# Kernel tuning notes

Hardware: AMD Instinct MI355X
Metric: run time of the kernel (lower is better)

The kernel has to match this reference:

```python
import jax, jax.numpy as jnp
import numpy as np

N_NODES = 50000
N_EDGES = 1600000
IN_FEAT = 256
OUT_FEAT = 64


def setup_inputs() -> dict:
    key = jax.random.key(0)
    k1, k2, k3, k4, k5, k6 = jax.random.split(key, 6)
    feat = jax.random.normal(k1, (N_NODES, IN_FEAT), dtype=jnp.float32)
    edge_src = jax.random.randint(k2, (N_EDGES,), 0, N_NODES, dtype=jnp.int32)
    edge_dst = jax.random.randint(k3, (N_EDGES,), 0, N_NODES, dtype=jnp.int32)
    edge_weight = jax.random.uniform(k4, (N_EDGES,), dtype=jnp.float32)
    # Xavier-uniform init as in reset_parameters
    bound = float(np.sqrt(6.0 / (IN_FEAT + OUT_FEAT)))
    W_self = jax.random.uniform(k5, (IN_FEAT, OUT_FEAT), minval=-bound, maxval=bound, dtype=jnp.float32)
    W_neigh = jax.random.uniform(k6, (IN_FEAT, OUT_FEAT), minval=-bound, maxval=bound, dtype=jnp.float32)
    return {"feat": feat, "edge_src": edge_src, "edge_dst": edge_dst,
            "edge_weight": edge_weight, "W_self": W_self, "W_neigh": W_neigh}


def reference(feat, edge_src, edge_dst, edge_weight, W_self, W_neigh):
    # neigh_feat = spmm(adj, feat): row dst aggregates weighted neighbors src
    gathered = feat[edge_src] * edge_weight[:, None]          # [E, in_feat]
    neigh_feat = jax.ops.segment_sum(gathered, edge_dst, num_segments=N_NODES)  # [N, in_feat]
    self_feat = feat @ W_self                                 # [N, out_feat]
    neigh_feat = neigh_feat @ W_neigh                         # [N, out_feat]
    out = jax.nn.relu(self_feat + neigh_feat)
    # dropout p=0.0 -> identity
    return out
```

## Files before the change

### kernel.cpp

```cpp
#include <hip/hip_runtime.h>

#define IN_FEAT 256
#define OUT_FEAT 64
#define BBITS2 6
#define GSZ 64
#define NB2 782
#define CAPB 2560
#define CNT_STRIDE 16
#define EPB 4096
#define SCT 512

typedef __attribute__((ext_vector_type(8))) short bf16x8;
typedef __attribute__((ext_vector_type(4))) float f32x4;

static __device__ __forceinline__ short f2bf(float f) {
    unsigned u = __float_as_uint(f);
    unsigned r = (u + 0x7FFFu + ((u >> 16) & 1u)) >> 16;
    return (short)r;
}
static __device__ __forceinline__ float bflo(unsigned v) {
    return __uint_as_float(v << 16);
}
static __device__ __forceinline__ float bfhi(unsigned v) {
    return __uint_as_float(v & 0xFFFF0000u);
}

__global__ __launch_bounds__(256) void prep(
    const float* __restrict__ Wself,
    const float* __restrict__ Wneigh,
    bf16x8* __restrict__ Wfrag,
    int* __restrict__ cnt, int cnt_words)
{
    const int t = blockIdx.x * 256 + threadIdx.x;
    if (t < 4096) {
        const int kstep = t >> 9;
        const int ntile = (t >> 6) & 7;
        const int lane  = t & 63;
        const int quad  = lane >> 4;
        const int n     = ntile * 16 + (lane & 15);
        const float* src = (n < OUT_FEAT) ? (Wself + n) : (Wneigh + (n - OUT_FEAT));
        const int k0 = kstep * 32 + quad * 8;
        bf16x8 v;
#pragma unroll
        for (int j = 0; j < 8; ++j) v[j] = f2bf(src[(size_t)(k0 + j) * OUT_FEAT]);
        Wfrag[t] = v;
    }
    const int nthr = gridDim.x * 256;
    for (int i = t; i < cnt_words; i += nthr) cnt[i] = 0;
}

__global__ __launch_bounds__(SCT) void gemm_scatter(
    const float* __restrict__ feat,
    const bf16x8* __restrict__ Wfrag,
    unsigned short* __restrict__ accSelf,
    unsigned short* __restrict__ Pn,
    const int* __restrict__ esrc,
    const int* __restrict__ edst,
    const float* __restrict__ ew,
    int* __restrict__ cnt,
    int2* __restrict__ binned,
    int n_nodes, int n_edges)
{
    __shared__ int  hist[NB2];
    __shared__ int  wsum[8];
    __shared__ int  loff[NB2];
    __shared__ int  lcur[NB2];
    __shared__ int  gbase[NB2];
    __shared__ int2 sorted[EPB];

    const int t    = threadIdx.x;
    const int wave = t >> 6;
    const int lane = t & 63;

    for (int i = t; i < NB2; i += SCT) hist[i] = 0;

    {
        const int row0 = (blockIdx.x * 8 + wave) * 16;
        if (row0 < n_nodes) {
            const int quad = lane >> 4;
            const int l15  = lane & 15;

            f32x4 c[8];
#pragma unroll
            for (int i = 0; i < 8; ++i) c[i] = (f32x4){0.f, 0.f, 0.f, 0.f};

            const int arow = min(row0 + l15, n_nodes - 1);
            const float* afeat = feat + (size_t)arow * IN_FEAT + quad * 8;

#pragma unroll
            for (int kstep = 0; kstep < 8; ++kstep) {
                const float4 x = *(const float4*)(afeat + kstep * 32);
                const float4 y = *(const float4*)(afeat + kstep * 32 + 4);
                bf16x8 a;
                a[0] = f2bf(x.x); a[1] = f2bf(x.y); a[2] = f2bf(x.z); a[3] = f2bf(x.w);
                a[4] = f2bf(y.x); a[5] = f2bf(y.y); a[6] = f2bf(y.z); a[7] = f2bf(y.w);
                bf16x8 b[8];
#pragma unroll
                for (int nt = 0; nt < 8; ++nt) b[nt] = Wfrag[(kstep * 8 + nt) * 64 + lane];
#pragma unroll
                for (int nt = 0; nt < 8; ++nt)
                    c[nt] = __builtin_amdgcn_mfma_f32_16x16x32_bf16(a, b[nt], c[nt], 0, 0, 0);
            }

#pragma unroll
            for (int nt = 0; nt < 8; ++nt) {
                unsigned short* dst = (nt < 4) ? accSelf : Pn;
                const int col = (nt & 3) * 16 + l15;
#pragma unroll
                for (int r = 0; r < 4; ++r) {
                    const int row = row0 + quad * 4 + r;
                    if (row < n_nodes)
                        dst[(size_t)row * OUT_FEAT + col] = (unsigned short)f2bf(c[nt][r]);
                }
            }
        }
    }
    __syncthreads();

    const long base = (long)blockIdx.x * EPB;
    int2 rec[8];
    int  bin[8];
    bool ok[8];
#pragma unroll
    for (int k = 0; k < 8; ++k) {
        const long idx = base + k * SCT + t;
        ok[k] = idx < n_edges;
        if (ok[k]) {
            const int d = edst[idx];
            rec[k] = make_int2((d << 16) | esrc[idx], __float_as_int(ew[idx]));
            bin[k] = d >> BBITS2;
            atomicAdd(&hist[bin[k]], 1);
        }
    }
    __syncthreads();

    int s2 = 0;
    if (t < 391) s2 = hist[2 * t] + hist[2 * t + 1];
    int incl = s2;
#pragma unroll
    for (int off = 1; off < 64; off <<= 1) {
        const int u = __shfl_up(incl, off, 64);
        if (lane >= off) incl += u;
    }
    if (lane == 63) wsum[wave] = incl;
    __syncthreads();
    int woff = 0;
#pragma unroll
    for (int w = 0; w < 7; ++w) woff += (w < wave) ? wsum[w] : 0;
    if (t < 391) {
        const int excl = woff + incl - s2;
        const int h0 = hist[2 * t], h1 = hist[2 * t + 1];
        loff[2 * t] = excl;          lcur[2 * t] = excl;
        loff[2 * t + 1] = excl + h0; lcur[2 * t + 1] = excl + h0;
        gbase[2 * t]     = h0 ? atomicAdd(&cnt[(size_t)(2 * t) * CNT_STRIDE], h0) : 0;
        gbase[2 * t + 1] = h1 ? atomicAdd(&cnt[(size_t)(2 * t + 1) * CNT_STRIDE], h1) : 0;
    }
    __syncthreads();

#pragma unroll
    for (int k = 0; k < 8; ++k)
        if (ok[k]) sorted[atomicAdd(&lcur[bin[k]], 1)] = rec[k];
    __syncthreads();

    const int tot = (int)min((long)EPB, n_edges - base);
    for (int i = t; i < tot; i += SCT) {
        const int2 p = sorted[i];
        const int b = ((unsigned)p.x >> 16) >> BBITS2;
        const int ofs = gbase[b] + (i - loff[b]);
        if (ofs < CAPB) binned[(size_t)b * CAPB + ofs] = p;
    }
}

__global__ __launch_bounds__(512) void bucket_gather(
    const int2* __restrict__ binned,
    const int* __restrict__ cnt,
    const unsigned short* __restrict__ Pn,
    const unsigned short* __restrict__ accSelf,
    float* __restrict__ out, int n_nodes)
{
    __shared__ unsigned sepk[CAPB];
    __shared__ int  hcnt[GSZ];
    __shared__ int  hoff[GSZ + 1];
    __shared__ int  hcur[GSZ];
    __shared__ int  snrec;

    const int b = blockIdx.x;
    const int t = threadIdx.x;

    if (t == 0) snrec = min(cnt[(size_t)b * CNT_STRIDE], CAPB);
    if (t < GSZ) hcnt[t] = 0;
    __syncthreads();
    const int nrec = snrec;
    const int2* rb = binned + (size_t)b * CAPB;

    int2 rc[5];
    int  dl[5];
    bool ok[5];
#pragma unroll
    for (int k = 0; k < 5; ++k) {
        const int i = k * 512 + t;
        ok[k] = i < nrec;
        if (ok[k]) {
            rc[k] = rb[i];
            dl[k] = ((unsigned)rc[k].x >> 16) & (GSZ - 1);
            atomicAdd(&hcnt[dl[k]], 1);
        }
    }
    __syncthreads();

    if (t < GSZ) {
        const int h = hcnt[t];
        int incl = h;
#pragma unroll
        for (int off = 1; off < 64; off <<= 1) {
            const int u = __shfl_up(incl, off, 64);
            if (t >= off) incl += u;
        }
        hoff[t] = incl - h;
        hcur[t] = incl - h;
        if (t == GSZ - 1) hoff[GSZ] = incl;
    }
    __syncthreads();

#pragma unroll
    for (int k = 0; k < 5; ++k) {
        if (ok[k]) {
            const int pos = atomicAdd(&hcur[dl[k]], 1);
            const unsigned wq = (unsigned)__float2int_rn(__int_as_float(rc[k].y) * 65535.0f);
            sepk[pos] = ((unsigned)rc[k].x & 0xFFFFu) | (wq << 16);
        }
    }
    __syncthreads();

    const int wv   = t >> 6;
    const int lane = t & 63;
    const int half = lane >> 5;
    const int c2   = (lane & 31) * 2;

#pragma unroll
    for (int ldn = wv * 8; ldn < wv * 8 + 8; ++ldn) {
        const int dst = b * GSZ + ldn;
        if (dst >= n_nodes) break;
        const int beg = hoff[ldn];
        const int end = hoff[ldn + 1];

        float A0[8], A1[8];
#pragma unroll
        for (int j = 0; j < 8; ++j) { A0[j] = 0.f; A1[j] = 0.f; }

        int e = beg + half;
        for (; e + 14 < end; e += 16) {
#pragma unroll
            for (int j = 0; j < 8; ++j) {
                const unsigned p = sepk[e + 2 * j];
                const unsigned v = *(const unsigned*)(Pn + (size_t)(p & 0xFFFFu) * OUT_FEAT + c2);
                const float w = (float)(p >> 16) * (1.0f / 65535.0f);
                A0[j] += w * bflo(v);
                A1[j] += w * bfhi(v);
            }
        }
        for (; e + 6 < end; e += 8) {
#pragma unroll
            for (int j = 0; j < 4; ++j) {
                const unsigned p = sepk[e + 2 * j];
                const unsigned v = *(const unsigned*)(Pn + (size_t)(p & 0xFFFFu) * OUT_FEAT + c2);
                const float w = (float)(p >> 16) * (1.0f / 65535.0f);
                A0[j] += w * bflo(v);
                A1[j] += w * bfhi(v);
            }
        }
        for (; e < end; e += 2) {
            const unsigned p = sepk[e];
            const unsigned v = *(const unsigned*)(Pn + (size_t)(p & 0xFFFFu) * OUT_FEAT + c2);
            const float w = (float)(p >> 16) * (1.0f / 65535.0f);
            A0[0] += w * bflo(v);
            A1[0] += w * bfhi(v);
        }
        float s0 = ((A0[0] + A0[1]) + (A0[2] + A0[3])) + ((A0[4] + A0[5]) + (A0[6] + A0[7]));
        float s1 = ((A1[0] + A1[1]) + (A1[2] + A1[3])) + ((A1[4] + A1[5]) + (A1[6] + A1[7]));
        s0 += __shfl_xor(s0, 32, 64);
        s1 += __shfl_xor(s1, 32, 64);
        if (half == 0) {
            const unsigned sv = *(const unsigned*)(accSelf + (size_t)dst * OUT_FEAT + c2);
            float2 o;
            o.x = fmaxf(bflo(sv) + s0, 0.f);
            o.y = fmaxf(bfhi(sv) + s1, 0.f);
            *(float2*)(out + (size_t)dst * OUT_FEAT + c2) = o;
        }
    }
}

extern "C" void kernel_launch(void* const* d_in, const int* in_sizes, int n_in,
                              void* d_out, int out_size, void* d_ws, size_t ws_size,
                              hipStream_t stream) {
    const float* feat   = (const float*)d_in[0];
    const int*   esrc   = (const int*)  d_in[1];
    const int*   edst   = (const int*)  d_in[2];
    const float* ew     = (const float*)d_in[3];
    const float* Wself  = (const float*)d_in[4];
    const float* Wneigh = (const float*)d_in[5];

    const int n_nodes = in_sizes[0] / IN_FEAT;
    const int n_edges = in_sizes[1];

    bf16x8* Wfrag           = (bf16x8*)d_ws;
    unsigned short* accSelf = (unsigned short*)((char*)d_ws + 65536);
    unsigned short* Pn      = accSelf + (size_t)n_nodes * OUT_FEAT;
    int2*  binned  = (int2*)(Pn + (size_t)n_nodes * OUT_FEAT);
    int*   cnt     = (int*)(binned + (size_t)NB2 * CAPB);
    float* out     = (float*)d_out;

    const int cnt_words = NB2 * CNT_STRIDE;
    prep<<<64, 256, 0, stream>>>(Wself, Wneigh, Wfrag, cnt, cnt_words);

    const int sblocks = (n_edges + EPB - 1) / EPB;
    const int tblocks = (((n_nodes + 15) / 16) + 7) / 8;
    const int fblocks = (sblocks > tblocks) ? sblocks : tblocks;
    gemm_scatter<<<fblocks, SCT, 0, stream>>>(
        feat, Wfrag, accSelf, Pn, esrc, edst, ew, cnt, binned, n_nodes, n_edges);

    bucket_gather<<<NB2, 512, 0, stream>>>(binned, cnt, Pn, accSelf, out, n_nodes);
}
```

Baseline: 176.4 us.

## Warp-specialize gemm_scatter: half waves do MFMA GEMM, half bin edges concurrently

Splits the 512-thread block so waves 0-3 each compute two 16-row GEMM tiles while waves 4-7 load edges and build per-wave shared histograms at the same time. Previously the GEMM and the edge loading ran one after the other, separated by a barrier. Using four private histograms also reduces LDS atomic contention. The cost is that each GEMM wave now does twice the work and each edge-loading thread holds 16 records in registers, which raises register pressure and may lower occupancy.

```diff
diff --git a/kernel.cpp b/kernel.cpp
--- a/kernel.cpp
+++ b/kernel.cpp
@@ -61,7 +61,7 @@
     int2* __restrict__ binned,
     int n_nodes, int n_edges)
 {
-    __shared__ int  hist[NB2];
+    __shared__ int  hist4[4][NB2];
     __shared__ int  wsum[8];
     __shared__ int  loff[NB2];
     __shared__ int  lcur[NB2];
@@ -71,76 +71,82 @@
     const int t    = threadIdx.x;
     const int wave = t >> 6;
     const int lane = t & 63;
-
-    for (int i = t; i < NB2; i += SCT) hist[i] = 0;
-
-    {
-        const int row0 = (blockIdx.x * 8 + wave) * 16;
-        if (row0 < n_nodes) {
-            const int quad = lane >> 4;
-            const int l15  = lane & 15;
-
-            f32x4 c[8];
-#pragma unroll
-            for (int i = 0; i < 8; ++i) c[i] = (f32x4){0.f, 0.f, 0.f, 0.f};
-
-            const int arow = min(row0 + l15, n_nodes - 1);
-            const float* afeat = feat + (size_t)arow * IN_FEAT + quad * 8;
-
-#pragma unroll
-            for (int kstep = 0; kstep < 8; ++kstep) {
-                const float4 x = *(const float4*)(afeat + kstep * 32);
-                const float4 y = *(const float4*)(afeat + kstep * 32 + 4);
-                bf16x8 a;
-                a[0] = f2bf(x.x); a[1] = f2bf(x.y); a[2] = f2bf(x.z); a[3] = f2bf(x.w);
-                a[4] = f2bf(y.x); a[5] = f2bf(y.y); a[6] = f2bf(y.z); a[7] = f2bf(y.w);
-                bf16x8 b[8];
-#pragma unroll
-                for (int nt = 0; nt < 8; ++nt) b[nt] = Wfrag[(kstep * 8 + nt) * 64 + lane];
-#pragma unroll
-                for (int nt = 0; nt < 8; ++nt)
-                    c[nt] = __builtin_amdgcn_mfma_f32_16x16x32_bf16(a, b[nt], c[nt], 0, 0, 0);
-            }
-
-#pragma unroll
-            for (int nt = 0; nt < 8; ++nt) {
-                unsigned short* dst = (nt < 4) ? accSelf : Pn;
-                const int col = (nt & 3) * 16 + l15;
-#pragma unroll
-                for (int r = 0; r < 4; ++r) {
-                    const int row = row0 + quad * 4 + r;
-                    if (row < n_nodes)
-                        dst[(size_t)row * OUT_FEAT + col] = (unsigned short)f2bf(c[nt][r]);
+    const long base = (long)blockIdx.x * EPB;
+
+    int2 rec[16];
+    bool ok[16];
+
+    if (wave < 4) {
+#pragma unroll
+        for (int j = 0; j < 2; ++j) {
+            const int row0 = (blockIdx.x * 8 + wave * 2 + j) * 16;
+            if (row0 < n_nodes) {
+                const int quad = lane >> 4;
+                const int l15  = lane & 15;
+
+                f32x4 c[8];
+#pragma unroll
+                for (int i = 0; i < 8; ++i) c[i] = (f32x4){0.f, 0.f, 0.f, 0.f};
+
+                const int arow = min(row0 + l15, n_nodes - 1);
+                const float* afeat = feat + (size_t)arow * IN_FEAT + quad * 8;
+
+#pragma unroll
+                for (int kstep = 0; kstep < 8; ++kstep) {
+                    const float4 x = *(const float4*)(afeat + kstep * 32);
+                    const float4 y = *(const float4*)(afeat + kstep * 32 + 4);
+                    bf16x8 a;
+                    a[0] = f2bf(x.x); a[1] = f2bf(x.y); a[2] = f2bf(x.z); a[3] = f2bf(x.w);
+                    a[4] = f2bf(y.x); a[5] = f2bf(y.y); a[6] = f2bf(y.z); a[7] = f2bf(y.w);
+                    bf16x8 b[8];
+#pragma unroll
+                    for (int nt = 0; nt < 8; ++nt) b[nt] = Wfrag[(kstep * 8 + nt) * 64 + lane];
+#pragma unroll
+                    for (int nt = 0; nt < 8; ++nt)
+                        c[nt] = __builtin_amdgcn_mfma_f32_16x16x32_bf16(a, b[nt], c[nt], 0, 0, 0);
                 }
-            }
-        }
-    }
-    __syncthreads();
-
-    const long base = (long)blockIdx.x * EPB;
-    int2 rec[8];
-    int  bin[8];
-    bool ok[8];
-#pragma unroll
-    for (int k = 0; k < 8; ++k) {
-        const long idx = base + k * SCT + t;
-        ok[k] = idx < n_edges;
-        if (ok[k]) {
-            const int d = edst[idx];
-            rec[k] = make_int2((d << 16) | esrc[idx], __float_as_int(ew[idx]));
-            bin[k] = d >> BBITS2;
-            atomicAdd(&hist[bin[k]], 1);
-        }
-    }
-    __syncthreads();
-
-    int s2 = 0;
-    if (t < 391) s2 = hist[2 * t] + hist[2 * t + 1];
+
+#pragma unroll
+                for (int nt = 0; nt < 8; ++nt) {
+                    unsigned short* dst = (nt < 4) ? accSelf : Pn;
+                    const int col = (nt & 3) * 16 + l15;
+#pragma unroll
+                    for (int r = 0; r < 4; ++r) {
+                        const int row = row0 + quad * 4 + r;
+                        if (row < n_nodes)
+                            dst[(size_t)row * OUT_FEAT + col] = (unsigned short)f2bf(c[nt][r]);
+                    }
+                }
+            }
+        }
+    } else {
+        const int sw = wave - 4;
+        for (int i = lane; i < NB2; i += 64) hist4[sw][i] = 0;
+        const int u = t - 256;
+#pragma unroll
+        for (int k = 0; k < 16; ++k) {
+            const long idx = base + k * 256 + u;
+            ok[k] = idx < n_edges;
+            if (ok[k]) {
+                const int d = edst[idx];
+                rec[k] = make_int2((d << 16) | esrc[idx], __float_as_int(ew[idx]));
+                atomicAdd(&hist4[sw][d >> BBITS2], 1);
+            }
+        }
+    }
+    __syncthreads();
+
+    int s2 = 0, h0 = 0, h1 = 0;
+    if (t < 391) {
+        h0 = hist4[0][2 * t] + hist4[1][2 * t] + hist4[2][2 * t] + hist4[3][2 * t];
+        h1 = hist4[0][2 * t + 1] + hist4[1][2 * t + 1] + hist4[2][2 * t + 1] + hist4[3][2 * t + 1];
+        s2 = h0 + h1;
+    }
     int incl = s2;
 #pragma unroll
     for (int off = 1; off < 64; off <<= 1) {
-        const int u = __shfl_up(incl, off, 64);
-        if (lane >= off) incl += u;
+        const int uu = __shfl_up(incl, off, 64);
+        if (lane >= off) incl += uu;
     }
     if (lane == 63) wsum[wave] = incl;
     __syncthreads();
@@ -149,7 +155,6 @@
     for (int w = 0; w < 7; ++w) woff += (w < wave) ? wsum[w] : 0;
     if (t < 391) {
         const int excl = woff + incl - s2;
-        const int h0 = hist[2 * t], h1 = hist[2 * t + 1];
         loff[2 * t] = excl;          lcur[2 * t] = excl;
         loff[2 * t + 1] = excl + h0; lcur[2 * t + 1] = excl + h0;
         gbase[2 * t]     = h0 ? atomicAdd(&cnt[(size_t)(2 * t) * CNT_STRIDE], h0) : 0;
@@ -157,9 +162,14 @@
     }
     __syncthreads();
 
-#pragma unroll
-    for (int k = 0; k < 8; ++k)
-        if (ok[k]) sorted[atomicAdd(&lcur[bin[k]], 1)] = rec[k];
+    if (wave >= 4) {
+#pragma unroll
+        for (int k = 0; k < 16; ++k)
+            if (ok[k]) {
+                const int b = ((unsigned)rec[k].x >> 16) >> BBITS2;
+                sorted[atomicAdd(&lcur[b], 1)] = rec[k];
+            }
+    }
     __syncthreads();
 
     const int tot = (int)min((long)EPB, n_edges - base);
```

Result: faster. 168.3 us, median of 2 (-4.6%).
